# Kernel tuning notes

Hardware: AMD Instinct MI355X
Metric: run time of the kernel (lower is better)

Reference implementation:

```python
import jax, jax.numpy as jnp
import numpy as np

N_UNITS = 100
N_INPUTS = 7
N_OUTPUTS = 1
T = 60
STIM_ON, STIM_OFF = 10, 15
RESP_START, RESP_END = 20, 35
REWARD_DURATION = 5
ALPHA = 0.2            # dt / tau = 100 / 500
SIGMA_REC = 0.15
B = 8192


def setup_inputs() -> dict:
    key = jax.random.key(0)
    k1, k2, k3, k4, k5, k6, k7 = jax.random.split(key, 7)
    W_in_raw = (jax.random.normal(k1, (N_UNITS, N_INPUTS)) * 0.05).astype(jnp.float32)
    W_rec_np = np.asarray(jax.random.normal(k2, (N_UNITS, N_UNITS))) / np.sqrt(N_UNITS)
    sr = float(np.abs(np.linalg.eigvals(W_rec_np)).max())
    W_rec = jnp.asarray(W_rec_np * (0.8 / sr), dtype=jnp.float32)
    b_rec = jnp.zeros((N_UNITS,), jnp.float32)
    w_out = (jax.random.normal(k3, (N_OUTPUTS, N_UNITS)) * 0.1).astype(jnp.float32)
    b_out = jnp.zeros((N_OUTPUTS,), jnp.float32)
    return {
        "y0": jnp.zeros((B, N_UNITS), jnp.float32),
        "noise": jax.random.normal(k4, (B, T, N_UNITS), dtype=jnp.float32),
        "stimulus_idx": jax.random.randint(k5, (B,), 0, 4).astype(jnp.int32),
        "rewarded_target_idx": jax.random.randint(k6, (B,), 0, 4).astype(jnp.int32),
        "instruction": jax.random.randint(k7, (B,), 0, 2).astype(jnp.int32),
        "W_in_raw": W_in_raw, "W_rec": W_rec, "b_rec": b_rec,
        "w_out": w_out, "b_out": b_out,
    }


def reference(y0, noise, stimulus_idx, rewarded_target_idx, instruction,
              W_in_raw, W_rec, b_rec, w_out, b_out):
    W_in = jnp.abs(W_in_raw)               # [N, n_in]
    w_lick = W_in[:, 5]
    w_reward = W_in[:, 4]
    noise_scale = SIGMA_REC * float(np.sqrt(2.0 * ALPHA))
    t_idx = jnp.arange(T, dtype=jnp.int32)
    stim_mask = ((t_idx >= STIM_ON) & (t_idx < STIM_OFF)).astype(jnp.float32)
    resp_mask = ((t_idx >= RESP_START) & (t_idx < RESP_END)).astype(jnp.float32)
    auto_start = RESP_END - REWARD_DURATION

    def trial(y0_i, eps_i, stim, rew, instr):
        is_rew = stim == rew
        instr_b = instr > 0
        # base open-loop input: stimulus channel + response cue (channel 6)
        u_base = jnp.zeros((T, N_INPUTS), jnp.float32).at[:, 6].set(resp_mask)
        u_base = u_base + stim_mask[:, None] * jax.nn.one_hot(stim, N_INPUTS, dtype=jnp.float32)
        wu = u_base @ W_in.T + b_rec        # [T, N]

        def step(carry, xs):
            y, licked, lick_t, instr_fired = carry
            t, wu_t, eps_t = xs
            # instruction auto-reward fires at auto_start if no reward yet (applied BEFORE pre)
            delivered = instr_fired | (licked & is_rew)
            fire = instr_b & (~delivered) & (t == auto_start)
            instr_fired = instr_fired | fire
            instr_active = instr_fired & (t >= auto_start) & (t < RESP_END)
            # lick-triggered inputs affect dynamics only AFTER the lick step (wu[t] already consumed)
            lick_dyn = licked & (t > lick_t) & (t < lick_t + REWARD_DURATION)
            add = (instr_active.astype(jnp.float32) + (lick_dyn & is_rew).astype(jnp.float32)) * w_reward \
                  + lick_dyn.astype(jnp.float32) * w_lick
            pre = y @ W_rec.T + wu_t + add + noise_scale * eps_t
            y = (1.0 - ALPHA) * y + ALPHA * jax.nn.relu(pre)
            z = jax.nn.sigmoid(y @ w_out.T + b_out)[0]
            # closed-loop lick decision (after readout)
            in_resp = (t >= RESP_START) & (t < RESP_END)
            trig = in_resp & (~licked) & (z > 0.5)
            lick_t = jnp.where(trig, t, lick_t)
            licked = licked | trig
            # u_trial markings include the lick step itself
            u5 = licked & (t >= lick_t) & (t < lick_t + REWARD_DURATION)
            u4 = instr_active | (u5 & is_rew)
            return (y, licked, lick_t, instr_fired), (z, u5, u4)

        init = (y0_i, jnp.array(False), jnp.array(T + 1, jnp.int32), jnp.array(False))
        (yf, licked, lick_t, instr_fired), (z_seq, u5, u4) = jax.lax.scan(
            step, init, (t_idx, wu, eps_i))
        u = u_base.at[:, 5].set(u5.astype(jnp.float32)).at[:, 4].set(u4.astype(jnp.float32))
        reward_delivered = instr_fired | (licked & is_rew)
        target = jnp.where(is_rew, resp_mask, jnp.zeros_like(resp_mask))
        return u, target, resp_mask > 0, licked, reward_delivered, z_seq, yf

    return jax.vmap(trial)(y0, noise, stimulus_idx, rewarded_target_idx, instruction)
```

## Files before the change

### kernel.cpp

```cpp
#include <hip/hip_runtime.h>
#include <math.h>

#define BB 8192
#define TT 60
#define NU 100
#define NI 7

typedef float v2f __attribute__((ext_vector_type(2)));

#define FOR50(M) M(0) M(1) M(2) M(3) M(4) M(5) M(6) M(7) M(8) M(9) \
  M(10) M(11) M(12) M(13) M(14) M(15) M(16) M(17) M(18) M(19) \
  M(20) M(21) M(22) M(23) M(24) M(25) M(26) M(27) M(28) M(29) \
  M(30) M(31) M(32) M(33) M(34) M(35) M(36) M(37) M(38) M(39) \
  M(40) M(41) M(42) M(43) M(44) M(45) M(46) M(47) M(48) M(49)

#define DECLW(sl) \
  const v2f wA_##sl = { W_rec[uao + 2*(sl)],     W_rec[ubo + 2*(sl)]     }; \
  const v2f wB_##sl = { W_rec[uao + 2*(sl) + 1], W_rec[ubo + 2*(sl) + 1] };

#define RL(v,l) __int_as_float(__builtin_amdgcn_readlane(__float_as_int(v), l))

#define MAC(sl) { \
  const float ya = RL(yy.x, sl); \
  const float yb = RL(yy.y, sl); \
  if ((sl) & 1) { accB0 += ya * wA_##sl; accB1 += yb * wB_##sl; } \
  else          { accA0 += ya * wA_##sl; accA1 += yb * wB_##sl; } }

#define DPPADD(ctrl, rmask) { \
  const int _t = __builtin_amdgcn_update_dpp(0, __float_as_int(part), (ctrl), (rmask), 0xf, false); \
  part += __int_as_float(_t); }

__global__ __launch_bounds__(256, 1)
void drr_kernel(const float* __restrict__ y0,
                const float* __restrict__ noise,
                const int*   __restrict__ stim_idx,
                const int*   __restrict__ rew_idx,
                const int*   __restrict__ instr_in,
                const float* __restrict__ W_in_raw,
                const float* __restrict__ W_rec,
                const float* __restrict__ b_rec,
                const float* __restrict__ w_out,
                const float* __restrict__ b_out,
                float* __restrict__ out)
{
    const int lane  = threadIdx.x & 63;
    const int wid   = threadIdx.x >> 6;
    const int trial = blockIdx.x * 4 + wid;

    const bool act = (lane < 50);
    const int  la  = act ? lane : 49;
    const int  ua  = 2 * la;
    const int  uao = ua * NU;
    const int  ubo = uao + NU;

    const int  stim    = stim_idx[trial];
    const int  rew     = rew_idx[trial];
    const bool is_rew  = (stim == rew);
    const bool instr_b = (instr_in[trial] > 0);

    FOR50(DECLW)

    const v2f wi6 = { fabsf(W_in_raw[ua * NI + 6]),    fabsf(W_in_raw[(ua+1) * NI + 6]) };
    const v2f wis = { fabsf(W_in_raw[ua * NI + stim]), fabsf(W_in_raw[(ua+1) * NI + stim]) };
    const v2f wr  = { fabsf(W_in_raw[ua * NI + 4]),    fabsf(W_in_raw[(ua+1) * NI + 4]) };
    const v2f wl  = { fabsf(W_in_raw[ua * NI + 5]),    fabsf(W_in_raw[(ua+1) * NI + 5]) };
    const v2f br  = { b_rec[ua], b_rec[ua + 1] };
    const v2f wo  = act ? (v2f){ w_out[ua], w_out[ua + 1] } : (v2f){ 0.0f, 0.0f };
    const float bo = b_out[0];

    const v2f* y0v = (const v2f*)(y0 + trial * NU);
    v2f yy = y0v[la];

    const float NS = 0.09486832980505138f;

    bool licked = false, instr_fired = false;
    int  lick_t = TT + 1;

    const float* nbase = noise + trial * (TT * NU);
    v2f en = ((const v2f*)nbase)[la];

    float* uout  = out;
    float* tout  = out  + BB * TT * NI;
    float* rout  = tout + BB * TT;
    float* lout  = rout + BB * TT;
    float* dout  = lout + BB;
    float* zout  = dout + BB;
    float* yfout = zout + BB * TT;

    for (int t = 0; t < TT; ++t) {
        const v2f e = en;
        if (t < TT - 1)
            en = ((const v2f*)(nbase + (t + 1) * NU))[la];

        const float sm = (t >= 10 && t < 15) ? 1.0f : 0.0f;
        const float rm = (t >= 20 && t < 35) ? 1.0f : 0.0f;

        const bool delivered    = instr_fired || (licked && is_rew);
        const bool fire         = instr_b && !delivered && (t == 30);
        instr_fired             = instr_fired || fire;
        const bool instr_active = instr_fired && (t >= 30) && (t < 35);
        const bool lick_dyn     = licked && (t > lick_t) && (t < lick_t + 5);
        const float a_rew  = (instr_active ? 1.0f : 0.0f) + ((lick_dyn && is_rew) ? 1.0f : 0.0f);
        const float a_lick = lick_dyn ? 1.0f : 0.0f;

        v2f accA0 = br + rm * wi6 + sm * wis + a_rew * wr + a_lick * wl + NS * e;
        v2f accA1 = { 0.0f, 0.0f };
        v2f accB0 = { 0.0f, 0.0f };
        v2f accB1 = { 0.0f, 0.0f };

        FOR50(MAC)

        const v2f pre = (accA0 + accA1) + (accB0 + accB1);
        const v2f prer = { fmaxf(pre.x, 0.0f), fmaxf(pre.y, 0.0f) };
        yy = 0.8f * yy + 0.2f * prer;

        float part = yy.x * wo.x + yy.y * wo.y;
        DPPADD(0x111, 0xf)
        DPPADD(0x112, 0xf)
        DPPADD(0x114, 0xf)
        DPPADD(0x118, 0xf)
        DPPADD(0x142, 0xa)
        DPPADD(0x143, 0xc)
        const float x = RL(part, 63) + bo;
        const float z = 1.0f / (1.0f + expf(-x));

        const bool in_resp = (t >= 20) && (t < 35);
        const bool trig    = in_resp && !licked && (z > 0.5f);
        if (trig) lick_t = t;
        licked = licked || trig;
        const bool u5 = licked && (t >= lick_t) && (t < lick_t + 5);
        const bool u4 = instr_active || (u5 && is_rew);

        const int bt = trial * TT + t;
        if (lane < NI) {
            float uv = 0.0f;
            if (lane == stim) uv = sm;
            if (lane == 4)    uv = u4 ? 1.0f : 0.0f;
            if (lane == 5)    uv = u5 ? 1.0f : 0.0f;
            if (lane == 6)    uv = rm;
            uout[bt * NI + lane] = uv;
        } else if (lane == 8) {
            tout[bt] = is_rew ? rm : 0.0f;
        } else if (lane == 9) {
            rout[bt] = rm;
        } else if (lane == 10) {
            zout[bt] = z;
        }
    }

    if (lane == 0) {
        lout[trial] = licked ? 1.0f : 0.0f;
        dout[trial] = (instr_fired || (licked && is_rew)) ? 1.0f : 0.0f;
    }
    if (act)
        ((v2f*)(yfout + trial * NU))[la] = yy;
}

extern "C" void kernel_launch(void* const* d_in, const int* in_sizes, int n_in,
                              void* d_out, int out_size, void* d_ws, size_t ws_size,
                              hipStream_t stream) {
    const float* y0       = (const float*)d_in[0];
    const float* noise    = (const float*)d_in[1];
    const int*   stim     = (const int*)  d_in[2];
    const int*   rew      = (const int*)  d_in[3];
    const int*   instr    = (const int*)  d_in[4];
    const float* W_in_raw = (const float*)d_in[5];
    const float* W_rec    = (const float*)d_in[6];
    const float* b_rec    = (const float*)d_in[7];
    const float* w_out    = (const float*)d_in[8];
    const float* b_out    = (const float*)d_in[9];
    float* out = (float*)d_out;

    drr_kernel<<<BB / 4, 256, 0, stream>>>(y0, noise, stim, rew, instr,
                                           W_in_raw, W_rec, b_rec, w_out, b_out, out);
}
```

Measured before the change: 584.7 us.

## Split each trial's recurrent matvec across two waves with LDS broadcast and exchange

Each trial now runs on two wavefronts. Each wave holds half of the K dimension of W_rec, 50 weights per lane instead of 100, and reads the broadcast hidden state from LDS with vector loads instead of scalar readlanes. The two partial sums are swapped through a double-buffered LDS array with one __syncthreads per step. This halves the serial MAC chain per wave and lowers register pressure so more waves can be resident, at the cost of a block barrier and LDS traffic on every timestep.

```diff
diff --git a/kernel.cpp b/kernel.cpp
--- a/kernel.cpp
+++ b/kernel.cpp
@@ -7,6 +7,8 @@
 #define NI 7
 
 typedef float v2f __attribute__((ext_vector_type(2)));
+typedef float v4f __attribute__((ext_vector_type(4)));
+
 
 #define FOR50(M) M(0) M(1) M(2) M(3) M(4) M(5) M(6) M(7) M(8) M(9) \
   M(10) M(11) M(12) M(13) M(14) M(15) M(16) M(17) M(18) M(19) \
@@ -14,23 +16,22 @@
   M(30) M(31) M(32) M(33) M(34) M(35) M(36) M(37) M(38) M(39) \
   M(40) M(41) M(42) M(43) M(44) M(45) M(46) M(47) M(48) M(49)
 
-#define DECLW(sl) \
-  const v2f wA_##sl = { W_rec[uao + 2*(sl)],     W_rec[ubo + 2*(sl)]     }; \
-  const v2f wB_##sl = { W_rec[uao + 2*(sl) + 1], W_rec[ubo + 2*(sl) + 1] };
+#define DECLW(j) const v2f w_##j = { W_rec[uaoff + kbase + (j)], W_rec[uboff + kbase + (j)] };
 
 #define RL(v,l) __int_as_float(__builtin_amdgcn_readlane(__float_as_int(v), l))
 
-#define MAC(sl) { \
-  const float ya = RL(yy.x, sl); \
-  const float yb = RL(yy.y, sl); \
-  if ((sl) & 1) { accB0 += ya * wA_##sl; accB1 += yb * wB_##sl; } \
-  else          { accA0 += ya * wA_##sl; accA1 += yb * wB_##sl; } }
+#define MACQ(q, wa, wb, wc, wd) { \
+  const v4f yq = *(const v4f*)(yb + 16*(q)); \
+  acc0 += wa * (v2f){yq.x, yq.x}; \
+  acc1 += wb * (v2f){yq.y, yq.y}; \
+  acc0 += wc * (v2f){yq.z, yq.z}; \
+  acc1 += wd * (v2f){yq.w, yq.w}; }
 
 #define DPPADD(ctrl, rmask) { \
   const int _t = __builtin_amdgcn_update_dpp(0, __float_as_int(part), (ctrl), (rmask), 0xf, false); \
   part += __int_as_float(_t); }
 
-__global__ __launch_bounds__(256, 1)
+__global__ __launch_bounds__(128, 4)
 void drr_kernel(const float* __restrict__ y0,
                 const float* __restrict__ noise,
                 const int*   __restrict__ stim_idx,
@@ -43,15 +44,19 @@
                 const float* __restrict__ b_out,
                 float* __restrict__ out)
 {
+    __shared__ __align__(16) float ybc[2][128];
+    __shared__ v2f pex[2][2][64];
+
     const int lane  = threadIdx.x & 63;
-    const int wid   = threadIdx.x >> 6;
-    const int trial = blockIdx.x * 4 + wid;
+    const int wid   = (threadIdx.x >> 6) & 1;
+    const int trial = blockIdx.x;
 
     const bool act = (lane < 50);
     const int  la  = act ? lane : 49;
     const int  ua  = 2 * la;
-    const int  uao = ua * NU;
-    const int  ubo = uao + NU;
+    const int  uaoff = ua * NU;
+    const int  uboff = uaoff + NU;
+    const int  kbase = wid * 50;
 
     const int  stim    = stim_idx[trial];
     const int  rew     = rew_idx[trial];
@@ -68,16 +73,18 @@
     const v2f wo  = act ? (v2f){ w_out[ua], w_out[ua + 1] } : (v2f){ 0.0f, 0.0f };
     const float bo = b_out[0];
 
-    const v2f* y0v = (const v2f*)(y0 + trial * NU);
-    v2f yy = y0v[la];
+    v2f yy = *(const v2f*)(y0 + trial * NU + ua);
 
     const float NS = 0.09486832980505138f;
 
     bool licked = false, instr_fired = false;
     int  lick_t = TT + 1;
 
-    const float* nbase = noise + trial * (TT * NU);
-    v2f en = ((const v2f*)nbase)[la];
+    const float* np = noise + trial * (TT * NU) + ua;
+    v2f en = *(const v2f*)np;
+
+    char* ybw = (char*)&ybc[wid][0] + (((ua + (wid ? 50 : 0)) % 100) * 4);
+    const char* yb = (const char*)&ybc[wid][0];
 
     float* uout  = out;
     float* tout  = out  + BB * TT * NI;
@@ -88,12 +95,11 @@
     float* yfout = zout + BB * TT;
 
     for (int t = 0; t < TT; ++t) {
+        *(v2f*)ybw = yy;
+
         const v2f e = en;
         if (t < TT - 1)
-            en = ((const v2f*)(nbase + (t + 1) * NU))[la];
-
-        const float sm = (t >= 10 && t < 15) ? 1.0f : 0.0f;
-        const float rm = (t >= 20 && t < 35) ? 1.0f : 0.0f;
+            en = *(const v2f*)(np + (t + 1) * NU);
 
         const bool delivered    = instr_fired || (licked && is_rew);
         const bool fire         = instr_b && !delivered && (t == 30);
@@ -103,16 +109,45 @@
         const float a_rew  = (instr_active ? 1.0f : 0.0f) + ((lick_dyn && is_rew) ? 1.0f : 0.0f);
         const float a_lick = lick_dyn ? 1.0f : 0.0f;
 
-        v2f accA0 = br + rm * wi6 + sm * wis + a_rew * wr + a_lick * wl + NS * e;
-        v2f accA1 = { 0.0f, 0.0f };
-        v2f accB0 = { 0.0f, 0.0f };
-        v2f accB1 = { 0.0f, 0.0f };
-
-        FOR50(MAC)
-
-        const v2f pre = (accA0 + accA1) + (accB0 + accB1);
-        const v2f prer = { fmaxf(pre.x, 0.0f), fmaxf(pre.y, 0.0f) };
-        yy = 0.8f * yy + 0.2f * prer;
+        const bool in_stim = (t >= 10) && (t < 15);
+        const bool in_resp = (t >= 20) && (t < 35);
+
+        v2f acc0 = { 0.0f, 0.0f };
+        v2f acc1 = { 0.0f, 0.0f };
+        MACQ(0,  w_0,  w_1,  w_2,  w_3)
+        MACQ(1,  w_4,  w_5,  w_6,  w_7)
+        MACQ(2,  w_8,  w_9,  w_10, w_11)
+        MACQ(3,  w_12, w_13, w_14, w_15)
+        MACQ(4,  w_16, w_17, w_18, w_19)
+        MACQ(5,  w_20, w_21, w_22, w_23)
+        MACQ(6,  w_24, w_25, w_26, w_27)
+        MACQ(7,  w_28, w_29, w_30, w_31)
+        MACQ(8,  w_32, w_33, w_34, w_35)
+        MACQ(9,  w_36, w_37, w_38, w_39)
+        MACQ(10, w_40, w_41, w_42, w_43)
+        MACQ(11, w_44, w_45, w_46, w_47)
+        { const v2f yp = *(const v2f*)(yb + 192);
+          acc0 += w_48 * (v2f){yp.x, yp.x};
+          acc1 += w_49 * (v2f){yp.y, yp.y}; }
+
+        const int par = t & 1;
+        const v2f pown = acc0 + acc1;
+        pex[par][wid][lane] = pown;
+        __syncthreads();
+        const v2f pothr = pex[par][wid ^ 1][lane];
+        const v2f plo = wid ? pothr : pown;
+        const v2f phi = wid ? pown  : pothr;
+
+        v2f base = br;
+        if (in_stim) base += wis;
+        if (in_resp) base += wi6;
+        if (a_rew  != 0.0f) base += (v2f){a_rew, a_rew} * wr;
+        if (a_lick != 0.0f) base += (v2f){a_lick, a_lick} * wl;
+        base += (v2f){NS, NS} * e;
+
+        v2f pre = base + (plo + phi);
+        pre = (v2f){ fmaxf(pre.x, 0.0f), fmaxf(pre.y, 0.0f) };
+        yy = (v2f){0.8f, 0.8f} * yy + (v2f){0.2f, 0.2f} * pre;
 
         float part = yy.x * wo.x + yy.y * wo.y;
         DPPADD(0x111, 0xf)
@@ -124,36 +159,42 @@
         const float x = RL(part, 63) + bo;
         const float z = 1.0f / (1.0f + expf(-x));
 
-        const bool in_resp = (t >= 20) && (t < 35);
-        const bool trig    = in_resp && !licked && (z > 0.5f);
+        const bool trig = in_resp && !licked && (z > 0.5f);
         if (trig) lick_t = t;
         licked = licked || trig;
         const bool u5 = licked && (t >= lick_t) && (t < lick_t + 5);
         const bool u4 = instr_active || (u5 && is_rew);
 
-        const int bt = trial * TT + t;
-        if (lane < NI) {
-            float uv = 0.0f;
-            if (lane == stim) uv = sm;
-            if (lane == 4)    uv = u4 ? 1.0f : 0.0f;
-            if (lane == 5)    uv = u5 ? 1.0f : 0.0f;
-            if (lane == 6)    uv = rm;
-            uout[bt * NI + lane] = uv;
-        } else if (lane == 8) {
-            tout[bt] = is_rew ? rm : 0.0f;
-        } else if (lane == 9) {
-            rout[bt] = rm;
-        } else if (lane == 10) {
-            zout[bt] = z;
+        const float sm = in_stim ? 1.0f : 0.0f;
+        const float rm = in_resp ? 1.0f : 0.0f;
+
+        if (!wid) {
+            const int bt = trial * TT + t;
+            if (lane < NI) {
+                float uv = 0.0f;
+                if (lane == stim) uv = sm;
+                if (lane == 4)    uv = u4 ? 1.0f : 0.0f;
+                if (lane == 5)    uv = u5 ? 1.0f : 0.0f;
+                if (lane == 6)    uv = rm;
+                uout[bt * NI + lane] = uv;
+            } else if (lane == 8) {
+                tout[bt] = is_rew ? rm : 0.0f;
+            } else if (lane == 9) {
+                rout[bt] = rm;
+            } else if (lane == 10) {
+                zout[bt] = z;
+            }
         }
     }
 
-    if (lane == 0) {
-        lout[trial] = licked ? 1.0f : 0.0f;
-        dout[trial] = (instr_fired || (licked && is_rew)) ? 1.0f : 0.0f;
+    if (!wid) {
+        if (lane == 0) {
+            lout[trial] = licked ? 1.0f : 0.0f;
+            dout[trial] = (instr_fired || (licked && is_rew)) ? 1.0f : 0.0f;
+        }
+        if (act)
+            *(v2f*)(yfout + trial * NU + ua) = yy;
     }
-    if (act)
-        ((v2f*)(yfout + trial * NU))[la] = yy;
 }
 
 extern "C" void kernel_launch(void* const* d_in, const int* in_sizes, int n_in,
@@ -171,6 +212,6 @@
     const float* b_out    = (const float*)d_in[9];
     float* out = (float*)d_out;
 
-    drr_kernel<<<BB / 4, 256, 0, stream>>>(y0, noise, stim, rew, instr,
-                                           W_in_raw, W_rec, b_rec, w_out, b_out, out);
+    drr_kernel<<<BB, 128, 0, stream>>>(y0, noise, stim, rew, instr,
+                                       W_in_raw, W_rec, b_rec, w_out, b_out, out);
 }
```

Result: slower. 827.0 us (+41.4%).
